# Kernel optimization log

Measured on AMD Instinct MI355X. Metric: run time of the kernel, lower is better.

## Reference

```python
import jax, jax.numpy as jnp
import numpy as np

B, N, C, CD, R = 8, 16384, 32, 256, 32


def setup_inputs() -> dict:
    key = jax.random.key(0)
    ks = jax.random.split(key, 12)
    f32 = jnp.float32
    p = lambda k, shape, s=0.05: jax.random.normal(k, shape, f32) * s
    return {
        "features": jax.random.normal(ks[0], (B, C, N), f32),
        "coords": jax.random.normal(ks[1], (B, 3, N), f32),
        "condition": jax.random.normal(ks[2], (B, CD), f32),
        "conv1_w": p(ks[3], (C, C, 3, 3, 3)), "conv1_b": jnp.zeros((C,), f32),
        "gn1_g": jnp.ones((C,), f32), "gn1_b": jnp.zeros((C,), f32),
        "mod1_w": p(ks[4], (2 * C, CD)),
        "mod1_b": jnp.concatenate([jnp.ones((C,)), jnp.zeros((C,))]).astype(f32),
        "conv2_w": p(ks[5], (C, C, 3, 3, 3)), "conv2_b": jnp.zeros((C,), f32),
        "gn2_g": jnp.ones((C,), f32), "gn2_b": jnp.zeros((C,), f32),
        "mod2_w": p(ks[6], (2 * C, CD)),
        "mod2_b": jnp.concatenate([jnp.ones((C,)), jnp.zeros((C,))]).astype(f32),
        "se_w1": p(ks[7], (C // 8, C)), "se_w2": p(ks[8], (C, C // 8)),
        "pc_w": p(ks[9], (C, C)), "pc_b": jnp.zeros((C,), f32),
        "gnp_g": jnp.ones((C,), f32), "gnp_b": jnp.zeros((C,), f32),
        "modp_w": p(ks[10], (2 * C, CD)),
        "modp_b": jnp.concatenate([jnp.ones((C,)), jnp.zeros((C,))]).astype(f32),
    }


def group_norm(x, g, b, G=8, eps=1e-5):
    shape = x.shape
    xg = x.reshape(shape[0], G, -1)
    m = xg.mean(-1, keepdims=True)
    v = xg.var(-1, keepdims=True)
    xn = ((xg - m) * jax.lax.rsqrt(v + eps)).reshape(shape)
    bshape = (1, shape[1]) + (1,) * (x.ndim - 2)
    return xn * g.reshape(bshape) + b.reshape(bshape)


def adagn(x, c, g, b, mw, mb):
    # GroupNorm then scale/shift from SiLU(c) @ Linear
    x = group_norm(x, g, b)
    m = jax.nn.silu(c) @ mw.T + mb  # (B, 2C)
    scale, shift = jnp.split(m, 2, axis=1)
    bshape = (x.shape[0], x.shape[1]) + (1,) * (x.ndim - 2)
    return x * scale.reshape(bshape) + shift.reshape(bshape)


def voxelize(features, coords, r):
    # scatter-average point features into r^3 grid; coords detached as in torch
    coords = jax.lax.stop_gradient(coords)
    nc = coords - coords.mean(2, keepdims=True)
    denom = jnp.max(jnp.linalg.norm(nc, axis=1, keepdims=True), axis=2, keepdims=True) * 2.0
    nc = nc / denom + 0.5
    nc = jnp.clip(nc * r, 0, r - 1)  # (B,3,N) continuous in [0, r-1]
    vc = jnp.round(nc).astype(jnp.int32)
    idx = (vc[:, 0] * r + vc[:, 1]) * r + vc[:, 2]  # (B,N) flat voxel ids

    def per_batch(f, i):
        s = jax.ops.segment_sum(f.T, i, num_segments=r ** 3)  # (V, D)
        cnt = jax.ops.segment_sum(jnp.ones(i.shape, f.dtype), i, num_segments=r ** 3)
        return (s / jnp.maximum(cnt, 1.0)[:, None]).T.reshape(f.shape[0], r, r, r)

    vox = jax.vmap(per_batch)(features, idx)  # (B, D, r, r, r)
    return vox, nc


def devoxelize(vox, coords, r):
    # trilinear gather of voxel features back to points
    Bv, D = vox.shape[:2]
    flat = vox.reshape(Bv, D, r * r * r)
    lo = jnp.floor(coords)
    frac = coords - lo
    lo = lo.astype(jnp.int32)
    hi = jnp.minimum(lo + 1, r - 1)
    gather = jax.vmap(lambda f, i: f[:, i])  # per-batch (D,V)[:, (N,)] -> (D,N)
    out = jnp.zeros((Bv, D, coords.shape[2]), vox.dtype)
    for dx in (0, 1):
        ix = hi[:, 0] if dx else lo[:, 0]
        wx = frac[:, 0] if dx else 1.0 - frac[:, 0]
        for dy in (0, 1):
            iy = hi[:, 1] if dy else lo[:, 1]
            wy = frac[:, 1] if dy else 1.0 - frac[:, 1]
            for dz in (0, 1):
                iz = hi[:, 2] if dz else lo[:, 2]
                wz = frac[:, 2] if dz else 1.0 - frac[:, 2]
                idx = (ix * r + iy) * r + iz
                out = out + gather(flat, idx) * (wx * wy * wz)[:, None, :]
    return out


def conv3d(x, w, b):
    y = jax.lax.conv_general_dilated(x, w, (1, 1, 1), 'SAME',
                                     dimension_numbers=('NCDHW', 'OIDHW', 'NCDHW'))
    return y + b[None, :, None, None, None]


def reference(features, coords, condition, conv1_w, conv1_b, gn1_g, gn1_b, mod1_w,
              mod1_b, conv2_w, conv2_b, gn2_g, gn2_b, mod2_w, mod2_b, se_w1, se_w2,
              pc_w, pc_b, gnp_g, gnp_b, modp_w, modp_b):
    vox, nc = voxelize(features, coords, R)
    v = conv3d(vox, conv1_w, conv1_b)
    v = jax.nn.silu(adagn(v, condition, gn1_g, gn1_b, mod1_w, mod1_b))
    v = conv3d(v, conv2_w, conv2_b)
    v = adagn(v, condition, gn2_g, gn2_b, mod2_w, mod2_b)
    # SE3d squeeze-excite
    s = jax.nn.sigmoid(jax.nn.relu(v.mean((2, 3, 4)) @ se_w1.T) @ se_w2.T)
    v = v * s[:, :, None, None, None]
    vfeat = devoxelize(v, nc, R)  # (B, C, N)
    # point branch: 1x1 conv + AdaGN + SiLU
    px = jnp.einsum('bdn,od->bon', features, pc_w) + pc_b[None, :, None]
    px = jax.nn.silu(adagn(px, condition, gnp_g, gnp_b, modp_w, modp_b))
    return vfeat + px
```

## Files before the change

### kernel.cpp

```cpp
#include <hip/hip_runtime.h>
#include <math.h>

#define DEV_INLINE __device__ __forceinline__

namespace {

typedef unsigned short u16;
typedef unsigned int u32;
typedef __attribute__((ext_vector_type(8))) short short8v;
typedef __attribute__((ext_vector_type(16))) float f32x16;

constexpr int Bn = 8, Cn = 32, Nn = 16384, Rn = 32, Vn = Rn * Rn * Rn;

DEV_INLINE float siluf(float x) { return x / (1.0f + __expf(-x)); }
DEV_INLINE float bf2f(u16 u) { union { u32 i; float f; } x; x.i = (u32)u << 16; return x.f; }
DEV_INLINE u16 f2bf(float f) {
  union { float f; u32 i; } x; x.f = f;
  return (u16)((x.i + 0x7FFFu + ((x.i >> 16) & 1u)) >> 16);
}
DEV_INLINE u32 pack2(float a, float b) { return (u32)f2bf(a) | ((u32)f2bf(b) << 16); }
DEV_INLINE void unpack8(uint4 u, float* f) {
  f[0] = bf2f(u.x & 0xffff); f[1] = bf2f(u.x >> 16);
  f[2] = bf2f(u.y & 0xffff); f[3] = bf2f(u.y >> 16);
  f[4] = bf2f(u.z & 0xffff); f[5] = bf2f(u.z >> 16);
  f[6] = bf2f(u.w & 0xffff); f[7] = bf2f(u.w >> 16);
}

__global__ void k_cpart1(const float* __restrict__ coords, float* __restrict__ csum) {
  int blk = blockIdx.x;
  int b = blk >> 3, s = blk & 7;
  int t = threadIdx.x;
  const float* cb = coords + (size_t)b * 3 * Nn;
  int n0 = s * 2048;
  float sx = 0.f, sy = 0.f, sz = 0.f;
  for (int n = n0 + t; n < n0 + 2048; n += 256) {
    sx += cb[n]; sy += cb[Nn + n]; sz += cb[2 * Nn + n];
  }
  #pragma unroll
  for (int m = 1; m <= 32; m <<= 1) {
    sx += __shfl_xor(sx, m); sy += __shfl_xor(sy, m); sz += __shfl_xor(sz, m);
  }
  __shared__ float rs[3][4];
  if ((t & 63) == 0) { rs[0][t >> 6] = sx; rs[1][t >> 6] = sy; rs[2][t >> 6] = sz; }
  __syncthreads();
  if (t < 3) atomicAdd(&csum[b * 4 + t], rs[t][0] + rs[t][1] + rs[t][2] + rs[t][3]);
}

__global__ void k_cpart2(const float* __restrict__ coords, const float* __restrict__ csum,
                         int* __restrict__ cmax) {
  int blk = blockIdx.x;
  int b = blk >> 3, s = blk & 7;
  int t = threadIdx.x;
  const float* cb = coords + (size_t)b * 3 * Nn;
  const float invn = 1.0f / (float)Nn;
  float mx = csum[b * 4] * invn, my = csum[b * 4 + 1] * invn, mz = csum[b * 4 + 2] * invn;
  int n0 = s * 2048;
  float mq = 0.f;
  for (int n = n0 + t; n < n0 + 2048; n += 256) {
    float x = cb[n] - mx, y = cb[Nn + n] - my, z = cb[2 * Nn + n] - mz;
    mq = fmaxf(mq, x * x + y * y + z * z);
  }
  #pragma unroll
  for (int m = 1; m <= 32; m <<= 1) mq = fmaxf(mq, __shfl_xor(mq, m));
  __shared__ float rm[4];
  if ((t & 63) == 0) rm[t >> 6] = mq;
  __syncthreads();
  if (t == 0) {
    float v = fmaxf(fmaxf(rm[0], rm[1]), fmaxf(rm[2], rm[3]));
    atomicMax(cmax + b, __float_as_int(v));
  }
}

__global__ void k_cfinal(const float* __restrict__ coords, const float* __restrict__ csum,
                         const int* __restrict__ cmax, float* __restrict__ nc,
                         int* __restrict__ vidx, int* __restrict__ hist) {
  int i = blockIdx.x * 256 + threadIdx.x;
  int b = i >> 14, n = i & (Nn - 1);
  const float* cb = coords + (size_t)b * 3 * Nn;
  const float invn = 1.0f / (float)Nn;
  float mx = csum[b * 4] * invn, my = csum[b * 4 + 1] * invn, mz = csum[b * 4 + 2] * invn;
  float inv = 1.0f / (2.0f * sqrtf(__int_as_float(cmax[b])));
  float x = (cb[n] - mx) * inv + 0.5f;
  float y = (cb[Nn + n] - my) * inv + 0.5f;
  float z = (cb[2 * Nn + n] - mz) * inv + 0.5f;
  x = fminf(fmaxf(x * (float)Rn, 0.f), (float)(Rn - 1));
  y = fminf(fmaxf(y * (float)Rn, 0.f), (float)(Rn - 1));
  z = fminf(fmaxf(z * (float)Rn, 0.f), (float)(Rn - 1));
  float* ncb = nc + (size_t)b * 3 * Nn;
  ncb[n] = x; ncb[Nn + n] = y; ncb[2 * Nn + n] = z;
  int vx = (int)rintf(x), vy = (int)rintf(y), vz = (int)rintf(z);
  int v = (vx * Rn + vy) * Rn + vz;
  vidx[i] = v;
  atomicAdd(&hist[b * Vn + v], 1);
}

__global__ __launch_bounds__(256, 2) void k_pxlin(
    const float* __restrict__ feat, const float* __restrict__ w,
    const float* __restrict__ bias, float* __restrict__ featT,
    u16* __restrict__ pxb) {
  __shared__ float lw[1024];
  __shared__ float lb[32];
  __shared__ float lbuf[256 * 33];
  int t = threadIdx.x;
  for (int i = t; i < 1024; i += 256) lw[i] = w[i];
  if (t < 32) lb[t] = bias[t];
  int blk = blockIdx.x;
  int b = blk >> 6, tile = blk & 63;
  int n0 = tile * 256, n = n0 + t;
  float fr[32];
  const float* fb = feat + (size_t)b * 32 * Nn + n;
  #pragma unroll
  for (int ci = 0; ci < 32; ++ci) {
    fr[ci] = fb[(size_t)ci * Nn];
    lbuf[t * 33 + ci] = fr[ci];
  }
  __syncthreads();
  float* ftb = featT + ((size_t)b * Nn + n0) * 32;
  #pragma unroll
  for (int j = 0; j < 32; ++j) {
    int idx = j * 256 + t;
    ftb[idx] = lbuf[(idx >> 5) * 33 + (idx & 31)];
  }
  __syncthreads();
  u32* lbu = reinterpret_cast<u32*>(lbuf);
  #pragma unroll
  for (int p2 = 0; p2 < 16; ++p2) {
    int co0 = p2 * 2;
    float a0 = lb[co0], a1 = lb[co0 + 1];
    #pragma unroll
    for (int ci = 0; ci < 32; ++ci) {
      a0 += lw[co0 * 32 + ci] * fr[ci];
      a1 += lw[(co0 + 1) * 32 + ci] * fr[ci];
    }
    lbu[t * 17 + p2] = pack2(a0, a1);
  }
  __syncthreads();
  u32* pxu = reinterpret_cast<u32*>(pxb) + ((size_t)b * Nn + n0) * 16;
  #pragma unroll
  for (int j = 0; j < 16; ++j) {
    int idx = j * 256 + t;
    pxu[idx] = lbu[(idx >> 4) * 17 + (idx & 15)];
  }
}

__global__ void k_scan1(const int* __restrict__ hist, int* __restrict__ offs,
                        int* __restrict__ bsum) {
  __shared__ int sd[256];
  int t = threadIdx.x, blk = blockIdx.x;
  int4 h = reinterpret_cast<const int4*>(hist)[blk * 256 + t];
  int s = h.x + h.y + h.z + h.w;
  sd[t] = s; __syncthreads();
  for (int off = 1; off < 256; off <<= 1) {
    int add = (t >= off) ? sd[t - off] : 0;
    __syncthreads();
    sd[t] += add;
    __syncthreads();
  }
  int excl = sd[t] - s;
  int4 o;
  o.x = excl; o.y = excl + h.x; o.z = o.y + h.y; o.w = o.z + h.z;
  reinterpret_cast<int4*>(offs)[blk * 256 + t] = o;
  if (t == 0) bsum[blk] = sd[255];
}

__global__ void k_scan2(const int* __restrict__ bsum, int* __restrict__ bbase) {
  __shared__ int sd[256];
  int t = threadIdx.x;
  int s = bsum[t];
  sd[t] = s; __syncthreads();
  for (int off = 1; off < 256; off <<= 1) {
    int add = (t >= off) ? sd[t - off] : 0;
    __syncthreads();
    sd[t] += add;
    __syncthreads();
  }
  bbase[t] = sd[t] - s;
}

__global__ void k_sortidx(const int* __restrict__ vidx, int* __restrict__ offs,
                          const int* __restrict__ bbase, int* __restrict__ pidx) {
  int i = blockIdx.x * 256 + threadIdx.x;
  int b = i >> 14, n = i & (Nn - 1);
  int g = b * Vn + vidx[i];
  int p = atomicAdd(&offs[g], 1) + bbase[g >> 10];
  pidx[p] = n;
}

__global__ void k_voxavg(const int* __restrict__ hist, const int* __restrict__ offs,
                         const int* __restrict__ bbase, const int* __restrict__ pidx,
                         const float* __restrict__ featT, uint2* __restrict__ vox0) {
  int t = threadIdx.x;
  int wv = blockIdx.x * 4 + (t >> 6);
  int lane = t & 63;
  int c4 = lane & 7, j = lane >> 3;
  int b = wv >> 15;
  int cnt = hist[wv];
  float ax = 0.f, ay = 0.f, az = 0.f, aw = 0.f;
  if (cnt > 0) {
    int end = offs[wv] + bbase[wv >> 10];
    int start = end - cnt;
    const float4* ft = reinterpret_cast<const float4*>(featT) + (size_t)b * Nn * 8;
    for (int k = start + j; k < end; k += 8) {
      int n = pidx[k];
      float4 v = ft[n * 8 + c4];
      ax += v.x; ay += v.y; az += v.z; aw += v.w;
    }
    #pragma unroll
    for (int m = 8; m <= 32; m <<= 1) {
      ax += __shfl_xor(ax, m); ay += __shfl_xor(ay, m);
      az += __shfl_xor(az, m); aw += __shfl_xor(aw, m);
    }
    float invc = 1.0f / (float)cnt;
    ax *= invc; ay *= invc; az *= invc; aw *= invc;
  }
  if (j == 0) {
    uint2 o;
    o.x = pack2(ax, ay);
    o.y = pack2(az, aw);
    vox0[(size_t)wv * 8 + c4] = o;
  }
}

__global__ void k_twz(const float* __restrict__ w, u16* __restrict__ wt) {
  int i = blockIdx.x * 256 + threadIdx.x;
  if (i >= 27 * 32 * 32) return;
  int e = i & 7, l = (i >> 3) & 63, h = (i >> 9) & 1, k = i >> 10;
  int co = l & 31, ci = h * 16 + ((l >> 5) << 3) + e;
  wt[i] = f2bf(w[(co * 32 + ci) * 27 + k]);
}

__global__ void k_mods(const float* __restrict__ cond,
                       const float* __restrict__ w1, const float* __restrict__ b1,
                       const float* __restrict__ w2, const float* __restrict__ b2,
                       const float* __restrict__ wp, const float* __restrict__ bp,
                       float* __restrict__ m1, float* __restrict__ m2,
                       float* __restrict__ mp) {
  int blk = blockIdx.x;
  int mat = blk >> 3, b = blk & 7;
  int t = threadIdx.x;
  __shared__ float sc[256];
  sc[t] = siluf(cond[b * 256 + t]);
  __syncthreads();
  const float* w = (mat == 0) ? w1 : ((mat == 1) ? w2 : wp);
  const float* bb = (mat == 0) ? b1 : ((mat == 1) ? b2 : bp);
  float* dst = (mat == 0) ? m1 : ((mat == 1) ? m2 : mp);
  int wave = t >> 6, lane = t & 63;
  const float4* w4 = reinterpret_cast<const float4*>(w);
  float4 sv = reinterpret_cast<const float4*>(sc)[lane];
  #pragma unroll
  for (int i = 0; i < 16; ++i) {
    int oo = wave * 16 + i;
    float4 wv = w4[oo * 64 + lane];
    float p = wv.x * sv.x + wv.y * sv.y + wv.z * sv.z + wv.w * sv.w;
    #pragma unroll
    for (int m = 1; m <= 32; m <<= 1) p += __shfl_xor(p, m);
    if (lane == 0) dst[b * 64 + oo] = p + bb[oo];
  }
}

template <bool AFF>
DEV_INLINE void stage_load(const u16* __restrict__ in, size_t bbase, int x, int ytn,
                           int t, const float* __restrict__ Ac,
                           const float* __restrict__ Bc, int b, uint4* sv) {
  #pragma unroll
  for (int it = 0; it < 5; ++it) {
    int i = it * 512 + t;
    uint4 val = make_uint4(0u, 0u, 0u, 0u);
    if (i < 2448) {
      int col = i / 136, rem = i - col * 136;
      int c4 = rem / 34, r = rem - c4 * 34;
      int dxp = col / 6, yy = col - dxp * 6;
      int gx = x + dxp - 1, gy = ytn * 4 + yy - 1, z = r - 1;
      if ((unsigned)gx < 32u && (unsigned)gy < 32u && (unsigned)z < 32u) {
        val = *reinterpret_cast<const uint4*>(
            in + (bbase + (size_t)((gx * 32 + gy) * 32 + z)) * 32 + c4 * 8);
        if (AFF) {
          float f[8];
          unpack8(val, f);
          float4 A0 = reinterpret_cast<const float4*>(Ac)[b * 8 + c4 * 2];
          float4 A1 = reinterpret_cast<const float4*>(Ac)[b * 8 + c4 * 2 + 1];
          float4 B0 = reinterpret_cast<const float4*>(Bc)[b * 8 + c4 * 2];
          float4 B1 = reinterpret_cast<const float4*>(Bc)[b * 8 + c4 * 2 + 1];
          f[0] = siluf(f[0] * A0.x + B0.x); f[1] = siluf(f[1] * A0.y + B0.y);
          f[2] = siluf(f[2] * A0.z + B0.z); f[3] = siluf(f[3] * A0.w + B0.w);
          f[4] = siluf(f[4] * A1.x + B1.x); f[5] = siluf(f[5] * A1.y + B1.y);
          f[6] = siluf(f[6] * A1.z + B1.z); f[7] = siluf(f[7] * A1.w + B1.w);
          val.x = pack2(f[0], f[1]); val.y = pack2(f[2], f[3]);
          val.z = pack2(f[4], f[5]); val.w = pack2(f[6], f[7]);
        }
      }
    }
    sv[it] = val;
  }
}

DEV_INLINE void stage_store(uint4* __restrict__ dst, int t, const uint4* sv) {
  #pragma unroll
  for (int it = 0; it < 5; ++it) {
    int i = it * 512 + t;
    if (i < 2448) dst[i] = sv[it];
  }
}

template <bool AFF>
__global__ __launch_bounds__(512, 2) void k_conv(
    const u16* __restrict__ in, const u16* __restrict__ wt,
    const float* __restrict__ bias, const float* __restrict__ Ac,
    const float* __restrict__ Bc, u16* __restrict__ out,
    float* __restrict__ pstat) {
  __shared__ uint4 lds_x[4896];
  __shared__ float red[4096];
  int t = threadIdx.x;
  int blk = blockIdx.x;
  int x = blk & 31, b = blk >> 5;
  size_t bbase = (size_t)b * Vn;
  int w = t >> 6, lane = t & 63;
  int ys = w >> 1, h = w & 1;
  int zc = lane & 31, hi = lane >> 5;

  short8v wreg[27];
  #pragma unroll
  for (int k = 0; k < 27; ++k)
    wreg[k] = *reinterpret_cast<const short8v*>(wt + ((size_t)(k * 2 + h) * 64 + lane) * 8);

  uint4 sv[5];
  stage_load<AFF>(in, bbase, x, 0, t, Ac, Bc, b, sv);
  stage_store(lds_x, t, sv);
  __syncthreads();

  float s16[16], q16[16];
  #pragma unroll
  for (int r = 0; r < 16; ++r) { s16[r] = 0.f; q16[r] = 0.f; }

  int cur = 0;
  for (int yt = 0; yt < 8; ++yt) {
    if (yt < 7) stage_load<AFF>(in, bbase, x, yt + 1, t, Ac, Bc, b, sv);

    f32x16 acc;
    #pragma unroll
    for (int r = 0; r < 16; ++r) acc[r] = 0.f;
    if (h == 0) {
      #pragma unroll
      for (int q = 0; q < 4; ++q) {
        float4 bq = *reinterpret_cast<const float4*>(bias + q * 8 + hi * 4);
        acc[q * 4 + 0] = bq.x; acc[q * 4 + 1] = bq.y;
        acc[q * 4 + 2] = bq.z; acc[q * 4 + 3] = bq.w;
      }
    }

    const u16* lx = reinterpret_cast<const u16*>(lds_x + cur * 2448);
    int cbase = 2 * h + hi;
    #pragma unroll
    for (int dxp = 0; dxp < 3; ++dxp) {
      #pragma unroll
      for (int dyp = 0; dyp < 3; ++dyp) {
        int col = dxp * 6 + ys + dyp;
        const u16* lcol = lx + ((col * 4 + cbase) * 34 + zc) * 8;
        #pragma unroll
        for (int dzp = 0; dzp < 3; ++dzp) {
          int k = (dxp * 3 + dyp) * 3 + dzp;
          short8v bb = *reinterpret_cast<const short8v*>(lcol + dzp * 8);
          acc = __builtin_amdgcn_mfma_f32_32x32x16_bf16(wreg[k], bb, acc, 0, 0, 0);
        }
      }
    }

    if (h == 1) {
      #pragma unroll
      for (int r = 0; r < 16; ++r) red[ys * 1024 + r * 64 + lane] = acc[r];
    }
    __syncthreads();
    if (h == 0) {
      #pragma unroll
      for (int r = 0; r < 16; ++r) acc[r] += red[ys * 1024 + r * 64 + lane];
      int y = yt * 4 + ys;
      size_t off = (bbase + (size_t)((x * 32 + y) * 32 + zc)) * 32;
      #pragma unroll
      for (int q = 0; q < 4; ++q) {
        uint2 o;
        o.x = pack2(acc[q * 4 + 0], acc[q * 4 + 1]);
        o.y = pack2(acc[q * 4 + 2], acc[q * 4 + 3]);
        *reinterpret_cast<uint2*>(out + off + q * 8 + hi * 4) = o;
      }
      #pragma unroll
      for (int r = 0; r < 16; ++r) { s16[r] += acc[r]; q16[r] += acc[r] * acc[r]; }
    }
    if (yt < 7) stage_store(lds_x + (cur ^ 1) * 2448, t, sv);
    __syncthreads();
    cur ^= 1;
  }

  if (h == 0) {
    #pragma unroll
    for (int m = 1; m <= 16; m <<= 1) {
      #pragma unroll
      for (int r = 0; r < 16; ++r) {
        s16[r] += __shfl_xor(s16[r], m);
        q16[r] += __shfl_xor(q16[r], m);
      }
    }
    if ((lane & 31) == 0) {
      #pragma unroll
      for (int r = 0; r < 16; ++r) {
        int co = (r & 3) + 8 * (r >> 2) + 4 * hi;
        red[ys * 64 + co] = s16[r];
        red[256 + ys * 64 + co] = q16[r];
      }
    }
  }
  __syncthreads();
  if (t < 64) {
    int arr = t >> 5, c = t & 31;
    const float* pr = red + arr * 256 + c;
    float v = pr[0] + pr[64] + pr[128] + pr[192];
    pstat[blk * 64 + arr * 32 + c] = v;
  }
}

__global__ void k_statspx(const u16* __restrict__ x, float* __restrict__ psum,
                          float* __restrict__ psq, int segs) {
  int blk = blockIdx.x;
  int b = blk / segs;
  int t = threadIdx.x;
  int c8 = t & 3, vsub = t >> 2;
  float s[8], q[8];
  #pragma unroll
  for (int j = 0; j < 8; ++j) { s[j] = 0.f; q[j] = 0.f; }
  const uint4* xb = reinterpret_cast<const uint4*>(x) + (size_t)blk * 4096;
  for (int it = 0; it < 16; ++it) {
    int v = it * 64 + vsub;
    uint4 u = xb[v * 4 + c8];
    float f[8];
    unpack8(u, f);
    #pragma unroll
    for (int j = 0; j < 8; ++j) { s[j] += f[j]; q[j] += f[j] * f[j]; }
  }
  #pragma unroll
  for (int m = 4; m <= 32; m <<= 1) {
    #pragma unroll
    for (int j = 0; j < 8; ++j) {
      s[j] += __shfl_xor(s[j], m);
      q[j] += __shfl_xor(q[j], m);
    }
  }
  __shared__ float ls[2][4][4][8];
  int wv = t >> 6;
  if ((t & 63) < 4) {
    #pragma unroll
    for (int j = 0; j < 8; ++j) { ls[0][wv][c8][j] = s[j]; ls[1][wv][c8][j] = q[j]; }
  }
  __syncthreads();
  if (t < 64) {
    int arr = t >> 5, c = t & 31;
    float v = ls[arr][0][c >> 3][c & 7] + ls[arr][1][c >> 3][c & 7] +
              ls[arr][2][c >> 3][c & 7] + ls[arr][3][c >> 3][c & 7];
    atomicAdd((arr == 0 ? psum : psq) + b * 32 + c, v);
  }
}

__global__ void k_coef1(const float* __restrict__ pstat, const float* __restrict__ mod,
                        const float* __restrict__ g, const float* __restrict__ bgn,
                        float* __restrict__ A, float* __restrict__ Bc) {
  int t = threadIdx.x;
  int b = t >> 5, c = t & 31;
  float cs = 0.f, cq = 0.f;
  const float* p = pstat + (size_t)b * 32 * 64;
  for (int i = 0; i < 32; ++i) {
    cs += p[i * 64 + c];
    cq += p[i * 64 + 32 + c];
  }
  __shared__ float ls[256], lq[256];
  ls[t] = cs; lq[t] = cq;
  __syncthreads();
  int gb = t & ~3;
  float s4 = ls[gb] + ls[gb + 1] + ls[gb + 2] + ls[gb + 3];
  float q4 = lq[gb] + lq[gb + 1] + lq[gb + 2] + lq[gb + 3];
  const float cntf = 4.0f * (float)Vn;
  float mean = s4 / cntf;
  float var = q4 / cntf - mean * mean;
  float rstd = rsqrtf(var + 1e-5f);
  float scale = mod[b * 64 + c], shift = mod[b * 64 + 32 + c];
  A[t] = rstd * g[c] * scale;
  Bc[t] = (bgn[c] - mean * rstd * g[c]) * scale + shift;
}

__global__ void k_coef2(const float* __restrict__ pstat, const float* __restrict__ mod,
                        const float* __restrict__ g, const float* __restrict__ bgn,
                        const float* __restrict__ sw1, const float* __restrict__ sw2,
                        float* __restrict__ S, float* __restrict__ T) {
  __shared__ float zm[8][32];
  __shared__ float hh[8][4];
  __shared__ float ls[256], lq[256];
  int t = threadIdx.x;
  int b = t >> 5, c = t & 31;
  float cs = 0.f, cq = 0.f;
  const float* p = pstat + (size_t)b * 32 * 64;
  for (int i = 0; i < 32; ++i) {
    cs += p[i * 64 + c];
    cq += p[i * 64 + 32 + c];
  }
  ls[t] = cs; lq[t] = cq;
  __syncthreads();
  int gb = t & ~3;
  float s4 = ls[gb] + ls[gb + 1] + ls[gb + 2] + ls[gb + 3];
  float q4 = lq[gb] + lq[gb + 1] + lq[gb + 2] + lq[gb + 3];
  const float cntf = 4.0f * (float)Vn;
  float mean = s4 / cntf;
  float var = q4 / cntf - mean * mean;
  float rstd = rsqrtf(var + 1e-5f);
  float scale = mod[b * 64 + c], shift = mod[b * 64 + 32 + c];
  float A = rstd * g[c] * scale;
  float Bv = (bgn[c] - mean * rstd * g[c]) * scale + shift;
  float chmean = cs / (float)Vn;
  zm[b][c] = A * chmean + Bv;
  __syncthreads();
  if (t < 32) {
    int b2 = t >> 2, j = t & 3;
    float hsum = 0;
    for (int cc = 0; cc < 32; ++cc) hsum += sw1[j * 32 + cc] * zm[b2][cc];
    hh[b2][j] = fmaxf(hsum, 0.f);
  }
  __syncthreads();
  float sig = 0;
  for (int j = 0; j < 4; ++j) sig += sw2[c * 4 + j] * hh[b][j];
  sig = 1.0f / (1.0f + __expf(-sig));
  S[t] = A * sig;
  T[t] = Bv * sig;
}

__global__ void k_coefp(const float* __restrict__ psum, const float* __restrict__ psq,
                        const float* __restrict__ mod, const float* __restrict__ g,
                        const float* __restrict__ bgn, float* __restrict__ A,
                        float* __restrict__ Bc) {
  __shared__ float ls[256], lq[256];
  int t = threadIdx.x;
  int b = t >> 5, c = t & 31;
  ls[t] = psum[t]; lq[t] = psq[t];
  __syncthreads();
  int gb = t & ~3;
  float s4 = ls[gb] + ls[gb + 1] + ls[gb + 2] + ls[gb + 3];
  float q4 = lq[gb] + lq[gb + 1] + lq[gb + 2] + lq[gb + 3];
  const float cntf = 4.0f * (float)Nn;
  float m = s4 / cntf;
  float var = q4 / cntf - m * m;
  float r = rsqrtf(var + 1e-5f);
  float scale = mod[b * 64 + c], shift = mod[b * 64 + 32 + c];
  A[t] = r * g[c] * scale;
  Bc[t] = (bgn[c] - m * r * g[c]) * scale + shift;
}

__global__ void k_devoxfinal(const u16* __restrict__ vox, const float* __restrict__ nc,
                             const u16* __restrict__ pxb, const float* __restrict__ S,
                             const float* __restrict__ T, const float* __restrict__ Ap,
                             const float* __restrict__ Bp, float* __restrict__ out) {
  int i = blockIdx.x * 256 + threadIdx.x;
  int b = i >> 14, n = i & (Nn - 1);
  const float* ncb = nc + (size_t)b * 3 * Nn;
  float fx = ncb[n], fy = ncb[Nn + n], fz = ncb[2 * Nn + n];
  float lxf = floorf(fx), lyf = floorf(fy), lzf = floorf(fz);
  float wx1 = fx - lxf, wy1 = fy - lyf, wz1 = fz - lzf;
  int lx = (int)lxf, ly = (int)lyf, lz = (int)lzf;
  int hx = min(lx + 1, 31), hy = min(ly + 1, 31), hz = min(lz + 1, 31);
  float a[32];
  #pragma unroll
  for (int c = 0; c < 32; ++c) a[c] = 0.f;
  for (int corner = 0; corner < 8; ++corner) {
    int cx = (corner & 4) ? hx : lx;
    int cy = (corner & 2) ? hy : ly;
    int cz = (corner & 1) ? hz : lz;
    float ww = ((corner & 4) ? wx1 : 1.f - wx1) *
               ((corner & 2) ? wy1 : 1.f - wy1) *
               ((corner & 1) ? wz1 : 1.f - wz1);
    const uint4* p = reinterpret_cast<const uint4*>(
        vox + ((size_t)b * Vn + (size_t)((cx * 32 + cy) * 32 + cz)) * 32);
    #pragma unroll
    for (int qq = 0; qq < 4; ++qq) {
      float f[8];
      unpack8(p[qq], f);
      #pragma unroll
      for (int j = 0; j < 8; ++j) a[qq * 8 + j] += ww * f[j];
    }
  }
  const uint4* pp = reinterpret_cast<const uint4*>(pxb) + (size_t)i * 4;
  float* o = out + (size_t)b * 32 * Nn + n;
  #pragma unroll
  for (int qq = 0; qq < 4; ++qq) {
    float pf[8];
    unpack8(pp[qq], pf);
    #pragma unroll
    for (int j = 0; j < 8; ++j) {
      int c = qq * 8 + j;
      float y = pf[j] * Ap[b * 32 + c] + Bp[b * 32 + c];
      o[(size_t)c * Nn] = a[c] * S[b * 32 + c] + T[b * 32 + c] + siluf(y);
    }
  }
}

}

extern "C" void kernel_launch(void* const* d_in, const int* in_sizes, int n_in,
                              void* d_out, int out_size, void* d_ws, size_t ws_size,
                              hipStream_t stream) {
  (void)in_sizes; (void)n_in; (void)out_size; (void)ws_size;
  const float* features = (const float*)d_in[0];
  const float* coords = (const float*)d_in[1];
  const float* condition = (const float*)d_in[2];
  const float* conv1_w = (const float*)d_in[3];
  const float* conv1_b = (const float*)d_in[4];
  const float* gn1_g = (const float*)d_in[5];
  const float* gn1_b = (const float*)d_in[6];
  const float* mod1_w = (const float*)d_in[7];
  const float* mod1_b = (const float*)d_in[8];
  const float* conv2_w = (const float*)d_in[9];
  const float* conv2_b = (const float*)d_in[10];
  const float* gn2_g = (const float*)d_in[11];
  const float* gn2_b = (const float*)d_in[12];
  const float* mod2_w = (const float*)d_in[13];
  const float* mod2_b = (const float*)d_in[14];
  const float* se_w1 = (const float*)d_in[15];
  const float* se_w2 = (const float*)d_in[16];
  const float* pc_w = (const float*)d_in[17];
  const float* pc_b = (const float*)d_in[18];
  const float* gnp_g = (const float*)d_in[19];
  const float* gnp_b = (const float*)d_in[20];
  const float* modp_w = (const float*)d_in[21];
  const float* modp_b = (const float*)d_in[22];

  char* w = (char*)d_ws;
  float* featT = (float*)w;
  u16* vox1 = (u16*)w;
  w += 16777216;
  u16* vox2 = (u16*)w; w += 16777216;
  u16* vox0 = (u16*)w; w += 16777216;
  u16* pxb = (u16*)w;  w += 8388608;
  int* hist = (int*)w;  w += 1048576;
  float* psump = (float*)w; w += 1024;
  float* psqp = (float*)w;  w += 1024;
  float* csum = (float*)w;  w += 128;
  int* cmax = (int*)w;      w += 64;
  int* offs = (int*)w;  w += 1048576;
  int* bsum = (int*)w;  w += 1024;
  int* bbase = (int*)w; w += 1024;
  int* pidx = (int*)w;  w += 524288;
  float* ncb = (float*)w;   w += 1572864;
  int* vidx = (int*)w;      w += 524288;
  u16* wt1b = (u16*)w;      w += 55296;
  u16* wt2b = (u16*)w;      w += 55296;
  float* pstat1 = (float*)w; w += 65536;
  float* pstat2 = (float*)w; w += 65536;
  float* m1 = (float*)w;    w += 2048;
  float* m2 = (float*)w;    w += 2048;
  float* mp = (float*)w;    w += 2048;
  float* A1 = (float*)w;    w += 1024;
  float* B1 = (float*)w;    w += 1024;
  float* Sc = (float*)w;    w += 1024;
  float* Tc = (float*)w;    w += 1024;
  float* Ap = (float*)w;    w += 1024;
  float* Bp = (float*)w;    w += 1024;
  float* out = (float*)d_out;

  hipMemsetAsync(hist, 0, 1048576 + 1024 + 1024 + 128 + 64, stream);

  k_pxlin<<<Bn * 64, 256, 0, stream>>>(features, pc_w, pc_b, featT, pxb);
  k_cpart1<<<Bn * 8, 256, 0, stream>>>(coords, csum);
  k_twz<<<108, 256, 0, stream>>>(conv1_w, wt1b);
  k_twz<<<108, 256, 0, stream>>>(conv2_w, wt2b);
  k_mods<<<24, 256, 0, stream>>>(condition, mod1_w, mod1_b, mod2_w, mod2_b,
                                 modp_w, modp_b, m1, m2, mp);
  k_statspx<<<Bn * 16, 256, 0, stream>>>(pxb, psump, psqp, 16);
  k_coefp<<<1, 256, 0, stream>>>(psump, psqp, mp, gnp_g, gnp_b, Ap, Bp);
  k_cpart2<<<Bn * 8, 256, 0, stream>>>(coords, csum, cmax);
  k_cfinal<<<(Bn * Nn) / 256, 256, 0, stream>>>(coords, csum, cmax, ncb, vidx, hist);
  k_scan1<<<256, 256, 0, stream>>>(hist, offs, bsum);
  k_scan2<<<1, 256, 0, stream>>>(bsum, bbase);
  k_sortidx<<<(Bn * Nn) / 256, 256, 0, stream>>>(vidx, offs, bbase, pidx);
  k_voxavg<<<(Bn * Vn) / 4, 256, 0, stream>>>(hist, offs, bbase, pidx, featT,
                                              (uint2*)vox0);
  k_conv<false><<<256, 512, 0, stream>>>(vox0, wt1b, conv1_b, nullptr, nullptr,
                                         vox1, pstat1);
  k_coef1<<<1, 256, 0, stream>>>(pstat1, m1, gn1_g, gn1_b, A1, B1);
  k_conv<true><<<256, 512, 0, stream>>>(vox1, wt2b, conv2_b, A1, B1, vox2, pstat2);
  k_coef2<<<1, 256, 0, stream>>>(pstat2, m2, gn2_g, gn2_b, se_w1, se_w2, Sc, Tc);
  k_devoxfinal<<<(Bn * Nn) / 256, 256, 0, stream>>>(vox2, ncb, pxb, Sc, Tc, Ap, Bp, out);
}
```

Measured before the change: 217.3 us.

## Split conv kernel into one block per y-tile, dropping in-block double buffering

The 3D conv kernel used to launch one block per (batch, x) slice and loop over eight y-tiles with a register-staged, double-buffered LDS pipeline. It now launches one block per (batch, x, y-tile), eight times as many blocks, each doing a single tile with a single LDS buffer and launch bounds raised to 4 blocks per CU. The goal is to fill the GPU's compute units, since 256 blocks underfill a large GPU, and to rely on occupancy for latency hiding. In exchange every block reloads the 27 weight registers, and the per-block GroupNorm partial stats grow eightfold, so the single-block coefficient kernels now loop over 256 partials instead of 32.

```diff
diff --git a/kernel.cpp b/kernel.cpp
--- a/kernel.cpp
+++ b/kernel.cpp
@@ -259,18 +259,35 @@
 }
 
 template <bool AFF>
-DEV_INLINE void stage_load(const u16* __restrict__ in, size_t bbase, int x, int ytn,
-                           int t, const float* __restrict__ Ac,
-                           const float* __restrict__ Bc, int b, uint4* sv) {
+__global__ __launch_bounds__(512, 4) void k_conv(
+    const u16* __restrict__ in, const u16* __restrict__ wt,
+    const float* __restrict__ bias, const float* __restrict__ Ac,
+    const float* __restrict__ Bc, u16* __restrict__ out,
+    float* __restrict__ pstat) {
+  __shared__ uint4 lds_x[2448];
+  __shared__ float red[4096];
+  int t = threadIdx.x;
+  int blk = blockIdx.x;
+  int yq = blk & 7, x = (blk >> 3) & 31, b = blk >> 8;
+  size_t bbase = (size_t)b * Vn;
+  int w = t >> 6, lane = t & 63;
+  int ys = w >> 1, h = w & 1;
+  int zc = lane & 31, hi = lane >> 5;
+
+  short8v wreg[27];
+  #pragma unroll
+  for (int k = 0; k < 27; ++k)
+    wreg[k] = *reinterpret_cast<const short8v*>(wt + ((size_t)(k * 2 + h) * 64 + lane) * 8);
+
   #pragma unroll
   for (int it = 0; it < 5; ++it) {
     int i = it * 512 + t;
-    uint4 val = make_uint4(0u, 0u, 0u, 0u);
     if (i < 2448) {
       int col = i / 136, rem = i - col * 136;
       int c4 = rem / 34, r = rem - c4 * 34;
       int dxp = col / 6, yy = col - dxp * 6;
-      int gx = x + dxp - 1, gy = ytn * 4 + yy - 1, z = r - 1;
+      int gx = x + dxp - 1, gy = yq * 4 + yy - 1, z = r - 1;
+      uint4 val = make_uint4(0u, 0u, 0u, 0u);
       if ((unsigned)gx < 32u && (unsigned)gy < 32u && (unsigned)z < 32u) {
         val = *reinterpret_cast<const uint4*>(
             in + (bbase + (size_t)((gx * 32 + gy) * 32 + z)) * 32 + c4 * 8);
@@ -289,108 +306,60 @@
           val.z = pack2(f[4], f[5]); val.w = pack2(f[6], f[7]);
         }
       }
-    }
-    sv[it] = val;
-  }
-}
-
-DEV_INLINE void stage_store(uint4* __restrict__ dst, int t, const uint4* sv) {
-  #pragma unroll
-  for (int it = 0; it < 5; ++it) {
-    int i = it * 512 + t;
-    if (i < 2448) dst[i] = sv[it];
-  }
-}
-
-template <bool AFF>
-__global__ __launch_bounds__(512, 2) void k_conv(
-    const u16* __restrict__ in, const u16* __restrict__ wt,
-    const float* __restrict__ bias, const float* __restrict__ Ac,
-    const float* __restrict__ Bc, u16* __restrict__ out,
-    float* __restrict__ pstat) {
-  __shared__ uint4 lds_x[4896];
-  __shared__ float red[4096];
-  int t = threadIdx.x;
-  int blk = blockIdx.x;
-  int x = blk & 31, b = blk >> 5;
-  size_t bbase = (size_t)b * Vn;
-  int w = t >> 6, lane = t & 63;
-  int ys = w >> 1, h = w & 1;
-  int zc = lane & 31, hi = lane >> 5;
-
-  short8v wreg[27];
-  #pragma unroll
-  for (int k = 0; k < 27; ++k)
-    wreg[k] = *reinterpret_cast<const short8v*>(wt + ((size_t)(k * 2 + h) * 64 + lane) * 8);
-
-  uint4 sv[5];
-  stage_load<AFF>(in, bbase, x, 0, t, Ac, Bc, b, sv);
-  stage_store(lds_x, t, sv);
-  __syncthreads();
-
+      lds_x[i] = val;
+    }
+  }
+  __syncthreads();
+
+  f32x16 acc;
+  #pragma unroll
+  for (int r = 0; r < 16; ++r) acc[r] = 0.f;
+  if (h == 0) {
+    #pragma unroll
+    for (int q = 0; q < 4; ++q) {
+      float4 bq = *reinterpret_cast<const float4*>(bias + q * 8 + hi * 4);
+      acc[q * 4 + 0] = bq.x; acc[q * 4 + 1] = bq.y;
+      acc[q * 4 + 2] = bq.z; acc[q * 4 + 3] = bq.w;
+    }
+  }
+
+  const u16* lx = reinterpret_cast<const u16*>(lds_x);
+  int cbase = 2 * h + hi;
+  #pragma unroll
+  for (int dxp = 0; dxp < 3; ++dxp) {
+    #pragma unroll
+    for (int dyp = 0; dyp < 3; ++dyp) {
+      int col = dxp * 6 + ys + dyp;
+      const u16* lcol = lx + ((col * 4 + cbase) * 34 + zc) * 8;
+      #pragma unroll
+      for (int dzp = 0; dzp < 3; ++dzp) {
+        int k = (dxp * 3 + dyp) * 3 + dzp;
+        short8v bb = *reinterpret_cast<const short8v*>(lcol + dzp * 8);
+        acc = __builtin_amdgcn_mfma_f32_32x32x16_bf16(wreg[k], bb, acc, 0, 0, 0);
+      }
+    }
+  }
+
+  if (h == 1) {
+    #pragma unroll
+    for (int r = 0; r < 16; ++r) red[ys * 1024 + r * 64 + lane] = acc[r];
+  }
+  __syncthreads();
   float s16[16], q16[16];
-  #pragma unroll
-  for (int r = 0; r < 16; ++r) { s16[r] = 0.f; q16[r] = 0.f; }
-
-  int cur = 0;
-  for (int yt = 0; yt < 8; ++yt) {
-    if (yt < 7) stage_load<AFF>(in, bbase, x, yt + 1, t, Ac, Bc, b, sv);
-
-    f32x16 acc;
-    #pragma unroll
-    for (int r = 0; r < 16; ++r) acc[r] = 0.f;
-    if (h == 0) {
-      #pragma unroll
-      for (int q = 0; q < 4; ++q) {
-        float4 bq = *reinterpret_cast<const float4*>(bias + q * 8 + hi * 4);
-        acc[q * 4 + 0] = bq.x; acc[q * 4 + 1] = bq.y;
-        acc[q * 4 + 2] = bq.z; acc[q * 4 + 3] = bq.w;
-      }
-    }
-
-    const u16* lx = reinterpret_cast<const u16*>(lds_x + cur * 2448);
-    int cbase = 2 * h + hi;
-    #pragma unroll
-    for (int dxp = 0; dxp < 3; ++dxp) {
-      #pragma unroll
-      for (int dyp = 0; dyp < 3; ++dyp) {
-        int col = dxp * 6 + ys + dyp;
-        const u16* lcol = lx + ((col * 4 + cbase) * 34 + zc) * 8;
-        #pragma unroll
-        for (int dzp = 0; dzp < 3; ++dzp) {
-          int k = (dxp * 3 + dyp) * 3 + dzp;
-          short8v bb = *reinterpret_cast<const short8v*>(lcol + dzp * 8);
-          acc = __builtin_amdgcn_mfma_f32_32x32x16_bf16(wreg[k], bb, acc, 0, 0, 0);
-        }
-      }
-    }
-
-    if (h == 1) {
-      #pragma unroll
-      for (int r = 0; r < 16; ++r) red[ys * 1024 + r * 64 + lane] = acc[r];
-    }
-    __syncthreads();
-    if (h == 0) {
-      #pragma unroll
-      for (int r = 0; r < 16; ++r) acc[r] += red[ys * 1024 + r * 64 + lane];
-      int y = yt * 4 + ys;
-      size_t off = (bbase + (size_t)((x * 32 + y) * 32 + zc)) * 32;
-      #pragma unroll
-      for (int q = 0; q < 4; ++q) {
-        uint2 o;
-        o.x = pack2(acc[q * 4 + 0], acc[q * 4 + 1]);
-        o.y = pack2(acc[q * 4 + 2], acc[q * 4 + 3]);
-        *reinterpret_cast<uint2*>(out + off + q * 8 + hi * 4) = o;
-      }
-      #pragma unroll
-      for (int r = 0; r < 16; ++r) { s16[r] += acc[r]; q16[r] += acc[r] * acc[r]; }
-    }
-    if (yt < 7) stage_store(lds_x + (cur ^ 1) * 2448, t, sv);
-    __syncthreads();
-    cur ^= 1;
-  }
-
   if (h == 0) {
+    #pragma unroll
+    for (int r = 0; r < 16; ++r) acc[r] += red[ys * 1024 + r * 64 + lane];
+    int y = yq * 4 + ys;
+    size_t off = (bbase + (size_t)((x * 32 + y) * 32 + zc)) * 32;
+    #pragma unroll
+    for (int q = 0; q < 4; ++q) {
+      uint2 o;
+      o.x = pack2(acc[q * 4 + 0], acc[q * 4 + 1]);
+      o.y = pack2(acc[q * 4 + 2], acc[q * 4 + 3]);
+      *reinterpret_cast<uint2*>(out + off + q * 8 + hi * 4) = o;
+    }
+    #pragma unroll
+    for (int r = 0; r < 16; ++r) { s16[r] = acc[r]; q16[r] = acc[r] * acc[r]; }
     #pragma unroll
     for (int m = 1; m <= 16; m <<= 1) {
       #pragma unroll
@@ -399,13 +368,14 @@
         q16[r] += __shfl_xor(q16[r], m);
       }
     }
-    if ((lane & 31) == 0) {
-      #pragma unroll
-      for (int r = 0; r < 16; ++r) {
-        int co = (r & 3) + 8 * (r >> 2) + 4 * hi;
-        red[ys * 64 + co] = s16[r];
-        red[256 + ys * 64 + co] = q16[r];
-      }
+  }
+  __syncthreads();
+  if (h == 0 && (lane & 31) == 0) {
+    #pragma unroll
+    for (int r = 0; r < 16; ++r) {
+      int co = (r & 3) + 8 * (r >> 2) + 4 * hi;
+      red[ys * 64 + co] = s16[r];
+      red[256 + ys * 64 + co] = q16[r];
     }
   }
   __syncthreads();
@@ -464,8 +434,8 @@
   int t = threadIdx.x;
   int b = t >> 5, c = t & 31;
   float cs = 0.f, cq = 0.f;
-  const float* p = pstat + (size_t)b * 32 * 64;
-  for (int i = 0; i < 32; ++i) {
+  const float* p = pstat + (size_t)b * 256 * 64;
+  for (int i = 0; i < 256; ++i) {
     cs += p[i * 64 + c];
     cq += p[i * 64 + 32 + c];
   }
@@ -494,8 +464,8 @@
   int t = threadIdx.x;
   int b = t >> 5, c = t & 31;
   float cs = 0.f, cq = 0.f;
-  const float* p = pstat + (size_t)b * 32 * 64;
-  for (int i = 0; i < 32; ++i) {
+  const float* p = pstat + (size_t)b * 256 * 64;
+  for (int i = 0; i < 256; ++i) {
     cs += p[i * 64 + c];
     cq += p[i * 64 + 32 + c];
   }
@@ -646,8 +616,8 @@
   int* vidx = (int*)w;      w += 524288;
   u16* wt1b = (u16*)w;      w += 55296;
   u16* wt2b = (u16*)w;      w += 55296;
-  float* pstat1 = (float*)w; w += 65536;
-  float* pstat2 = (float*)w; w += 65536;
+  float* pstat1 = (float*)w; w += 524288;
+  float* pstat2 = (float*)w; w += 524288;
   float* m1 = (float*)w;    w += 2048;
   float* m2 = (float*)w;    w += 2048;
   float* mp = (float*)w;    w += 2048;
@@ -676,10 +646,10 @@
   k_sortidx<<<(Bn * Nn) / 256, 256, 0, stream>>>(vidx, offs, bbase, pidx);
   k_voxavg<<<(Bn * Vn) / 4, 256, 0, stream>>>(hist, offs, bbase, pidx, featT,
                                               (uint2*)vox0);
-  k_conv<false><<<256, 512, 0, stream>>>(vox0, wt1b, conv1_b, nullptr, nullptr,
-                                         vox1, pstat1);
+  k_conv<false><<<2048, 512, 0, stream>>>(vox0, wt1b, conv1_b, nullptr, nullptr,
+                                          vox1, pstat1);
   k_coef1<<<1, 256, 0, stream>>>(pstat1, m1, gn1_g, gn1_b, A1, B1);
-  k_conv<true><<<256, 512, 0, stream>>>(vox1, wt2b, conv2_b, A1, B1, vox2, pstat2);
+  k_conv<true><<<2048, 512, 0, stream>>>(vox1, wt2b, conv2_b, A1, B1, vox2, pstat2);
   k_coef2<<<1, 256, 0, stream>>>(pstat2, m2, gn2_g, gn2_b, se_w1, se_w2, Sc, Tc);
   k_devoxfinal<<<(Bn * Nn) / 256, 256, 0, stream>>>(vox2, ncb, pxb, Sc, Tc, Ap, Bp, out);
 }
```

Result: slower. 261.6 us (+20.4%).
